# Kernel tuning notes

Hardware: AMD Instinct MI355X
Metric: run time of the kernel (lower is better)

The kernel has to match this reference:

```python
import jax, jax.numpy as jnp
import numpy as np

N, M = 8192, 1024  # n_frames, feature dim (input_size == output_size == 1024)
Q_SCALE = 0.06
DROP_P = 0.5


def setup_inputs() -> dict:
    key = jax.random.key(0)
    kx, kk, kq, kv, ko, ku = jax.random.split(key, 6)
    w_std = 0.02
    return {
        "x": jax.random.normal(kx, (N, M), dtype=jnp.float32),
        # nn.Linear stores weight as [out_features, in_features]
        "Wk": jax.random.normal(kk, (M, M), dtype=jnp.float32) * w_std,
        "Wq": jax.random.normal(kq, (M, M), dtype=jnp.float32) * w_std,
        "Wv": jax.random.normal(kv, (M, M), dtype=jnp.float32) * w_std,
        "Wo": jax.random.normal(ko, (M, M), dtype=jnp.float32) * w_std,
        # uniform noise for dropout mask on the [N, N] attention matrix
        "u": jax.random.uniform(ku, (N, N), dtype=jnp.float32),
    }


def reference(x, Wk, Wq, Wv, Wo, u):
    # projections (bias-free Linear: y = x @ W.T)
    K = x @ Wk.T                      # [N, M]
    Q = (x @ Wq.T) * Q_SCALE          # [N, M], Q *= 0.06
    V = x @ Wv.T                      # [N, M]
    logits = Q @ K.T                  # [N, N]
    attn = jax.nn.softmax(logits, axis=-1)
    # Dropout(p=0.5) in train mode: keep with prob 0.5, scale by 1/(1-p)=2
    keep = jnp.where(u >= DROP_P, jnp.float32(1.0 / (1.0 - DROP_P)), jnp.float32(0.0))
    w = attn * keep                   # [N, N]
    y = w @ V                         # [N, M]
    return y @ Wo.T                   # [N, M]
```

## Files before the change

### kernel.cpp

```cpp
#include <hip/hip_runtime.h>
#include <cstdint>
#include <cstddef>

#define NFRAMES 8192
#define MDIM    1024
#define Q_SCALE 0.06f

#define BK 64
#define BM2 256
#define BN2 256
#define BM 256
#define BN 128

typedef __bf16 bf16x8 __attribute__((ext_vector_type(8)));
typedef float  f32x4  __attribute__((ext_vector_type(4)));
typedef unsigned short us8 __attribute__((ext_vector_type(8)));

__device__ __forceinline__ unsigned short f2bf(float f) {
  union { float f; uint32_t u; } a; a.f = f;
  uint32_t u = a.u;
  u += 0x7FFFu + ((u >> 16) & 1u);
  return (unsigned short)(u >> 16);
}
__device__ __forceinline__ float bf2f(unsigned short h) {
  union { uint32_t u; float f; } a; a.u = ((uint32_t)h) << 16; return a.f;
}

__device__ __forceinline__ void async_ld16(const void* g, void* l) {
  __builtin_amdgcn_global_load_lds(
      (const __attribute__((address_space(1))) void*)(uintptr_t)g,
      (__attribute__((address_space(3))) void*)(uint32_t)(uintptr_t)l,
      16, 0, 0);
}

__device__ __forceinline__ void store_val(float* p, float v) { *p = v; }
__device__ __forceinline__ void store_val(unsigned short* p, float v) { *p = f2bf(v); }

template <typename OutT>
__global__ __launch_bounds__(512, 2) void gemm_big(
    const unsigned short* __restrict__ A, int lda,
    const unsigned short* __restrict__ B, int ldb,
    OutT* __restrict__ C, int ldc, long cz, int kChunk)
{
  __shared__ alignas(16) unsigned short As[2 * BM2 * BK];
  __shared__ alignas(16) unsigned short Bs[2 * BN2 * BK];

  const int tid  = threadIdx.x;
  const int wave = tid >> 6;
  const int lane = tid & 63;

  const int gX  = (int)gridDim.x;
  const int nwg = gX * (int)gridDim.y;
  int bx = (int)blockIdx.x, by = (int)blockIdx.y;
  if ((nwg & 7) == 0) {
    const int L  = by * gX + bx;
    const int qq = nwg >> 3;
    const int Ls = (L & 7) * qq + (L >> 3);
    bx = Ls % gX; by = Ls / gX;
  }

  const int m0 = by * BM2, n0 = bx * BN2;
  const int wm = (wave >> 2) * 128;
  const int wn = (wave & 3) * 64;
  const int fr = lane & 15, fq = lane >> 4;

  const int kOff = (int)blockIdx.z * kChunk;
  OutT* Cz = C + (size_t)blockIdx.z * cz;

  const int l8 = lane >> 3, l7 = lane & 7;
  const size_t ldaB = (size_t)lda * 2, ldbB = (size_t)ldb * 2;
  const char* aSrc = (const char*)A + (size_t)(m0 + wave * 8 + l8) * ldaB
                     + (size_t)kOff * 2 + ((l7 ^ l8) << 4);
  const char* bSrc = (const char*)B + (size_t)(n0 + wave * 8 + l8) * ldbB
                     + (size_t)kOff * 2 + ((l7 ^ l8) << 4);
  unsigned short* aDst = As + wave * 512;
  unsigned short* bDst = Bs + wave * 512;

  const int xorv = (fr & 7) << 4;
  const int c0 = (fq * 16) ^ xorv;
  const int c1 = (64 + fq * 16) ^ xorv;
  const char* aRd = (const char*)As + (wm + fr) * 128;
  const char* bRd = (const char*)Bs + (wn + fr) * 128;

  f32x4 acc[8][4] = {};
  const int NT = kChunk >> 6;

#define STA2(buf, s, t) async_ld16(aSrc + (size_t)((s) * 64) * ldaB + (size_t)(t) * 128, \
                                   aDst + (buf) * 16384 + (s) * 4096)
#define STB2(buf, s, t) async_ld16(bSrc + (size_t)((s) * 64) * ldbB + (size_t)(t) * 128, \
                                   bDst + (buf) * 16384 + (s) * 4096)

  STA2(0, 0, 0); STA2(0, 1, 0); STA2(0, 2, 0); STA2(0, 3, 0);
  STB2(0, 0, 0); STB2(0, 1, 0); STB2(0, 2, 0); STB2(0, 3, 0);
  asm volatile("s_waitcnt vmcnt(0)" ::: "memory");
  __builtin_amdgcn_s_barrier();

  for (int t = 0; t < NT; ++t) {
    const int cur = t & 1;
    const bool st = (t + 1 < NT);
    const char* aB = aRd + cur * 32768;
    const char* bB = bRd + cur * 32768;

    if (st) {
      const int u = t + 1, ub = cur ^ 1;
      STA2(ub, 0, u); STA2(ub, 1, u); STA2(ub, 2, u); STA2(ub, 3, u);
      STB2(ub, 0, u); STB2(ub, 1, u); STB2(ub, 2, u); STB2(ub, 3, u);
    }
    __builtin_amdgcn_sched_barrier(0);

    bf16x8 bh[4][2];
#pragma unroll
    for (int j = 0; j < 4; ++j) {
      bh[j][0] = *(const bf16x8*)(bB + j * 2048 + c0);
      bh[j][1] = *(const bf16x8*)(bB + j * 2048 + c1);
    }
    bf16x8 ar[2][2][2];
#pragma unroll
    for (int i = 0; i < 2; ++i) {
      ar[0][i][0] = *(const bf16x8*)(aB + i * 2048 + c0);
      ar[0][i][1] = *(const bf16x8*)(aB + i * 2048 + c1);
    }

#pragma unroll
    for (int ph = 0; ph < 4; ++ph) {
      const int pc = ph & 1, pn = pc ^ 1;
      if (ph < 3) {
#pragma unroll
        for (int i = 0; i < 2; ++i) {
          ar[pn][i][0] = *(const bf16x8*)(aB + (ph * 2 + 2 + i) * 2048 + c0);
          ar[pn][i][1] = *(const bf16x8*)(aB + (ph * 2 + 2 + i) * 2048 + c1);
        }
      }
      __builtin_amdgcn_s_setprio(1);
#pragma unroll
      for (int kk = 0; kk < 2; ++kk)
#pragma unroll
        for (int i = 0; i < 2; ++i)
#pragma unroll
          for (int j = 0; j < 4; ++j)
            acc[ph * 2 + i][j] = __builtin_amdgcn_mfma_f32_16x16x32_bf16(
                ar[pc][i][kk], bh[j][kk], acc[ph * 2 + i][j], 0, 0, 0);
      __builtin_amdgcn_s_setprio(0);
    }

    if (st) { asm volatile("s_waitcnt vmcnt(0)" ::: "memory"); }
    __builtin_amdgcn_s_barrier();
  }
#undef STA2
#undef STB2

#pragma unroll
  for (int mf = 0; mf < 8; ++mf)
#pragma unroll
    for (int nf = 0; nf < 4; ++nf)
#pragma unroll
      for (int r = 0; r < 4; ++r) {
        int row = m0 + wm + mf * 16 + fq * 4 + r;
        int col = n0 + wn + nf * 16 + fr;
        store_val(&Cz[(size_t)row * ldc + col], acc[mf][nf][r]);
      }
}

template <typename OutT>
__global__ __launch_bounds__(512, 2) void gemm_bt8(
    const unsigned short* __restrict__ A, int lda,
    const unsigned short* __restrict__ B, int ldb,
    OutT* __restrict__ C, int ldc, int K)
{
  __shared__ alignas(16) unsigned short As[3 * BM * BK];
  __shared__ alignas(16) unsigned short Bs[3 * BN * BK];

  const int tid  = threadIdx.x;
  const int wave = tid >> 6;
  const int lane = tid & 63;

  const int gX  = (int)gridDim.x;
  const int nwg = gX * (int)gridDim.y;
  const int L   = (int)blockIdx.y * gX + (int)blockIdx.x;
  const int qq  = nwg >> 3;
  const int Ls  = (L & 7) * qq + (L >> 3);
  const int bx  = Ls % gX, by = Ls / gX;

  const int m0 = by * BM, n0 = bx * BN;
  const int wm = (wave >> 1) * 64;
  const int wn = (wave & 1) * 64;
  const int fr = lane & 15, fq = lane >> 4;

  const int l8 = lane >> 3, l7 = lane & 7;
  const size_t ldaB = (size_t)lda * 2, ldbB = (size_t)ldb * 2;
  const char* aSrc = (const char*)A + (size_t)(m0 + wave * 8 + l8) * ldaB + ((l7 ^ l8) << 4);
  const char* bSrc = (const char*)B + (size_t)(n0 + wave * 8 + l8) * ldbB + ((l7 ^ l8) << 4);
  unsigned short* aDst = As + wave * 512;
  unsigned short* bDst = Bs + wave * 512;

  const int xorv = (fr & 7) << 4;
  const int cA0 = (fq * 16) ^ xorv;
  const int cA1 = (64 + fq * 16) ^ xorv;
  const char* aRd = (const char*)As + (wm + fr) * 128;
  const char* bRd = (const char*)Bs + (wn + fr) * 128;

  f32x4 acc[4][4] = {};
  const int NT = K >> 6;

#define STA(buf, s, t) async_ld16(aSrc + (size_t)((s) * 64) * ldaB + (size_t)(t) * 128, \
                                  aDst + (buf) * 16384 + (s) * 4096)
#define STB(buf, s, t) async_ld16(bSrc + (size_t)((s) * 64) * ldbB + (size_t)(t) * 128, \
                                  bDst + (buf) * 8192 + (s) * 4096)

  STA(0, 0, 0); STA(0, 1, 0); STA(0, 2, 0); STA(0, 3, 0); STB(0, 0, 0); STB(0, 1, 0);
  if (NT > 1) { STA(1, 0, 1); STA(1, 1, 1); STA(1, 2, 1); STA(1, 3, 1); STB(1, 0, 1); STB(1, 1, 1); }
  asm volatile("s_waitcnt vmcnt(6)" ::: "memory");
  __builtin_amdgcn_s_barrier();

  for (int t = 0; t < NT; ++t) {
    const int cur = t % 3;
    const int u   = t + 2;
    const int ub  = u % 3;
    const bool st = (u < NT);
    const char* aB = aRd + cur * 32768;
    const char* bB = bRd + cur * 16384;

    bf16x8 bh[4][2];
#pragma unroll
    for (int j = 0; j < 4; ++j) {
      bh[j][0] = *(const bf16x8*)(bB + j * 2048 + cA0);
      bh[j][1] = *(const bf16x8*)(bB + j * 2048 + cA1);
    }
    bf16x8 a0[2][2];
#pragma unroll
    for (int i = 0; i < 2; ++i) {
      a0[i][0] = *(const bf16x8*)(aB + i * 2048 + cA0);
      a0[i][1] = *(const bf16x8*)(aB + i * 2048 + cA1);
    }
    if (st) { STA(ub, 0, u); STA(ub, 1, u); STB(ub, 0, u); }
    __builtin_amdgcn_s_barrier();
    asm volatile("s_waitcnt lgkmcnt(0)" ::: "memory");
    __builtin_amdgcn_sched_barrier(0);
    __builtin_amdgcn_s_setprio(1);
#pragma unroll
    for (int kk = 0; kk < 2; ++kk)
#pragma unroll
      for (int i = 0; i < 2; ++i)
#pragma unroll
        for (int j = 0; j < 4; ++j)
          acc[i][j] = __builtin_amdgcn_mfma_f32_16x16x32_bf16(
              kk ? a0[i][1] : a0[i][0], kk ? bh[j][1] : bh[j][0], acc[i][j], 0, 0, 0);
    __builtin_amdgcn_s_setprio(0);
    __builtin_amdgcn_s_barrier();

    bf16x8 a1[2][2];
#pragma unroll
    for (int i = 0; i < 2; ++i) {
      a1[i][0] = *(const bf16x8*)(aB + (2 + i) * 2048 + cA0);
      a1[i][1] = *(const bf16x8*)(aB + (2 + i) * 2048 + cA1);
    }
    if (st) { STA(ub, 2, u); STA(ub, 3, u); STB(ub, 1, u); }
    if (st) { asm volatile("s_waitcnt vmcnt(6)" ::: "memory"); }
    else    { asm volatile("s_waitcnt vmcnt(0)" ::: "memory"); }
    __builtin_amdgcn_s_barrier();
    asm volatile("s_waitcnt lgkmcnt(0)" ::: "memory");
    __builtin_amdgcn_sched_barrier(0);
    __builtin_amdgcn_s_setprio(1);
#pragma unroll
    for (int kk = 0; kk < 2; ++kk)
#pragma unroll
      for (int i = 0; i < 2; ++i)
#pragma unroll
        for (int j = 0; j < 4; ++j)
          acc[2 + i][j] = __builtin_amdgcn_mfma_f32_16x16x32_bf16(
              kk ? a1[i][1] : a1[i][0], kk ? bh[j][1] : bh[j][0], acc[2 + i][j], 0, 0, 0);
    __builtin_amdgcn_s_setprio(0);
    __builtin_amdgcn_s_barrier();
  }
#undef STA
#undef STB

#pragma unroll
  for (int i = 0; i < 4; ++i)
#pragma unroll
    for (int j = 0; j < 4; ++j)
#pragma unroll
      for (int r = 0; r < 4; ++r) {
        int row = m0 + wm + i * 16 + fq * 4 + r;
        int col = n0 + wn + j * 16 + fr;
        store_val(&C[(size_t)row * ldc + col], acc[i][j][r]);
      }
}

__global__ __launch_bounds__(256) void softmax_dropout_kernel(
    const unsigned short* __restrict__ S, const float* __restrict__ U,
    unsigned short* __restrict__ P)
{
  const int row = blockIdx.x;
  const us8*   s8 = (const us8*)(S + (size_t)row * NFRAMES);
  const f32x4* u4 = (const f32x4*)(U + (size_t)row * NFRAMES);
  us8*         p8 = (us8*)(P + (size_t)row * NFRAMES);
  const int tid = threadIdx.x;
  const int lane = tid & 63, wave = tid >> 6;

  float v[32];
  float mx = -3.4e38f;
#pragma unroll
  for (int j = 0; j < 4; ++j) {
    us8 t = __builtin_nontemporal_load(s8 + j * 256 + tid);
#pragma unroll
    for (int e = 0; e < 8; ++e) {
      float f = bf2f(t[e]);
      v[j * 8 + e] = f;
      mx = fmaxf(mx, f);
    }
  }
#pragma unroll
  for (int o = 32; o > 0; o >>= 1) mx = fmaxf(mx, __shfl_xor(mx, o));
  __shared__ float redm[4];
  __shared__ float reds[4];
  if (lane == 0) redm[wave] = mx;
  __syncthreads();
  mx = fmaxf(fmaxf(redm[0], redm[1]), fmaxf(redm[2], redm[3]));

  float sum = 0.f;
#pragma unroll
  for (int i = 0; i < 32; ++i) { v[i] = __expf(v[i] - mx); sum += v[i]; }
#pragma unroll
  for (int o = 32; o > 0; o >>= 1) sum += __shfl_xor(sum, o);
  if (lane == 0) reds[wave] = sum;
  __syncthreads();
  sum = reds[0] + reds[1] + reds[2] + reds[3];
  float inv = 1.0f / sum;

#pragma unroll
  for (int j = 0; j < 4; ++j) {
    f32x4 ua = __builtin_nontemporal_load(u4 + (j * 256 + tid) * 2);
    f32x4 ub = __builtin_nontemporal_load(u4 + (j * 256 + tid) * 2 + 1);
    us8 o;
    o[0] = f2bf(v[j*8+0] * inv * (ua[0] >= 0.5f ? 2.0f : 0.0f));
    o[1] = f2bf(v[j*8+1] * inv * (ua[1] >= 0.5f ? 2.0f : 0.0f));
    o[2] = f2bf(v[j*8+2] * inv * (ua[2] >= 0.5f ? 2.0f : 0.0f));
    o[3] = f2bf(v[j*8+3] * inv * (ua[3] >= 0.5f ? 2.0f : 0.0f));
    o[4] = f2bf(v[j*8+4] * inv * (ub[0] >= 0.5f ? 2.0f : 0.0f));
    o[5] = f2bf(v[j*8+5] * inv * (ub[1] >= 0.5f ? 2.0f : 0.0f));
    o[6] = f2bf(v[j*8+6] * inv * (ub[2] >= 0.5f ? 2.0f : 0.0f));
    o[7] = f2bf(v[j*8+7] * inv * (ub[3] >= 0.5f ? 2.0f : 0.0f));
    p8[j * 256 + tid] = o;
  }
}

__device__ __forceinline__ void cvt4(const float* in, unsigned short* out, int i, float s) {
  float4 t = ((const float4*)in)[i];
  ushort4 o;
  o.x = f2bf(t.x * s); o.y = f2bf(t.y * s); o.z = f2bf(t.z * s); o.w = f2bf(t.w * s);
  ((ushort4*)out)[i] = o;
}

__global__ __launch_bounds__(256) void cvt_all(
    const float* __restrict__ x, const float* __restrict__ Wk,
    const float* __restrict__ Wq, const float* __restrict__ Wv,
    const float* __restrict__ Wo,
    unsigned short* __restrict__ xb, unsigned short* __restrict__ wkq,
    unsigned short* __restrict__ wvb, unsigned short* __restrict__ wob)
{
  int i = blockIdx.x * 256 + threadIdx.x;
  const int XSZ = (NFRAMES * MDIM) / 4;
  const int WSZ = (MDIM * MDIM) / 4;
  if (i < XSZ) { cvt4(x, xb, i, 1.0f); return; }
  i -= XSZ;
  if (i < WSZ) { cvt4(Wk, wkq, i, 1.0f); return; }
  i -= WSZ;
  if (i < WSZ) { cvt4(Wq, wkq + MDIM * MDIM, i, Q_SCALE); return; }
  i -= WSZ;
  if (i < WSZ) { cvt4(Wv, wvb, i, 1.0f); return; }
  i -= WSZ;
  if (i < WSZ) { cvt4(Wo, wob, i, 1.0f); return; }
}

__global__ __launch_bounds__(256) void reduce2_bf16(
    const float* __restrict__ Yp, long zs,
    unsigned short* __restrict__ out, int n4)
{
  int i = blockIdx.x * 256 + threadIdx.x;
  if (i < n4) {
    f32x4 a = __builtin_nontemporal_load((const f32x4*)Yp + i);
    f32x4 b = __builtin_nontemporal_load((const f32x4*)(Yp + zs) + i);
    ushort4 o;
    o.x = f2bf(a[0] + b[0]);
    o.y = f2bf(a[1] + b[1]);
    o.z = f2bf(a[2] + b[2]);
    o.w = f2bf(a[3] + b[3]);
    ((ushort4*)out)[i] = o;
  }
}

extern "C" void kernel_launch(void* const* d_in, const int* in_sizes, int n_in,
                              void* d_out, int out_size, void* d_ws, size_t ws_size,
                              hipStream_t stream) {
  const float* x  = (const float*)d_in[0];
  const float* Wk = (const float*)d_in[1];
  const float* Wq = (const float*)d_in[2];
  const float* Wv = (const float*)d_in[3];
  const float* Wo = (const float*)d_in[4];
  const float* u  = (const float*)d_in[5];
  float* out = (float*)d_out;

  const int N = NFRAMES, M = MDIM;
  char* base = (char*)d_ws;
  size_t off = 0;
  auto alloc = [&](size_t bytes) -> void* {
    void* p = base + off; off += (bytes + 255) & ~(size_t)255; return p;
  };
  unsigned short* xb  = (unsigned short*)alloc((size_t)N * M * 2);
  unsigned short* wkq = (unsigned short*)alloc((size_t)2 * M * M * 2);
  unsigned short* wvb = (unsigned short*)alloc((size_t)M * M * 2);
  unsigned short* wob = (unsigned short*)alloc((size_t)M * M * 2);
  unsigned short* KQb = (unsigned short*)alloc((size_t)N * 2 * M * 2);
  unsigned short* Vt  = (unsigned short*)alloc((size_t)M * N * 2);
  unsigned short* yb  = (unsigned short*)alloc((size_t)N * M * 2);

  size_t avail = ws_size > off ? ws_size - off : 0;
  int R = 256;
  const int cands[6] = {8192, 4096, 2048, 1024, 512, 256};
  for (int ci = 0; ci < 6; ++ci) {
    size_t need = (size_t)cands[ci] * N * 2 * 2 + 1024;
    if (need <= avail) { R = cands[ci]; break; }
  }
  unsigned short* Sb = (unsigned short*)alloc((size_t)R * N * 2);
  unsigned short* Pb = (unsigned short*)alloc((size_t)R * N * 2);
  float* Yp = (float*)Sb;

  {
    int total4 = (N * M + 4 * M * M) / 4;
    cvt_all<<<(total4 + 255) / 256, 256, 0, stream>>>(x, Wk, Wq, Wv, Wo, xb, wkq, wvb, wob);
  }

  gemm_big<unsigned short><<<dim3(2 * M / BN2, N / BM2), 512, 0, stream>>>(
      xb, M, wkq, M, KQb, 2 * M, 0, M);
  gemm_bt8<unsigned short><<<dim3(N / BN, M / BM), 512, 0, stream>>>(
      wvb, M, xb, M, Vt, N, M);

  for (int i0 = 0; i0 < N; i0 += R) {
    gemm_big<unsigned short><<<dim3(N / BN2, R / BM2), 512, 0, stream>>>(
        KQb + M + (size_t)i0 * 2 * M, 2 * M,
        KQb, 2 * M,
        Sb, N, 0, M);
    softmax_dropout_kernel<<<R, 256, 0, stream>>>(Sb, u + (size_t)i0 * N, Pb);
    gemm_big<float><<<dim3(M / BN2, R / BM2, 2), 512, 0, stream>>>(
        Pb, N, Vt, N, Yp, M, (long)R * M, N / 2);
    reduce2_bf16<<<(R * M / 4 + 255) / 256, 256, 0, stream>>>(
        Yp, (long)R * M, yb + (size_t)i0 * M, R * M / 4);
  }

  gemm_bt8<float><<<dim3(M / BN, N / BM), 512, 0, stream>>>(
      yb, M, wob, M, out, M, M);
}
```

Baseline: 716.8 us.

## Rewrite 256x256 GEMM main loop as 8-phase interleaved load/MFMA schedule

Replaces the double-buffered K loop of the big GEMM with an 8-phase schedule that unrolls two K tiles per iteration. Each phase issues part of the next tile's global-to-LDS loads, then runs a quarter of the MFMA block (4x2 fragments) between barriers. vmcnt(4) waits keep some prefetch in flight instead of draining it every tile. The goal is to overlap memory traffic with matrix math more finely, at the cost of many more barriers and an assumption that NT is even.

```diff
diff --git a/kernel.cpp b/kernel.cpp
--- a/kernel.cpp
+++ b/kernel.cpp
@@ -37,7 +37,7 @@
 __device__ __forceinline__ void store_val(unsigned short* p, float v) { *p = f2bf(v); }
 
 template <typename OutT>
-__global__ __launch_bounds__(512, 2) void gemm_big(
+__global__ __launch_bounds__(512, 2) void gemm_8ph(
     const unsigned short* __restrict__ A, int lda,
     const unsigned short* __restrict__ B, int ldb,
     OutT* __restrict__ C, int ldc, long cz, int kChunk)
@@ -73,81 +73,124 @@
                      + (size_t)kOff * 2 + ((l7 ^ l8) << 4);
   const char* bSrc = (const char*)B + (size_t)(n0 + wave * 8 + l8) * ldbB
                      + (size_t)kOff * 2 + ((l7 ^ l8) << 4);
-  unsigned short* aDst = As + wave * 512;
-  unsigned short* bDst = Bs + wave * 512;
 
   const int xorv = (fr & 7) << 4;
   const int c0 = (fq * 16) ^ xorv;
   const int c1 = (64 + fq * 16) ^ xorv;
   const char* aRd = (const char*)As + (wm + fr) * 128;
   const char* bRd = (const char*)Bs + (wn + fr) * 128;
+  const char* aB0 = aRd;
+  const char* aB1 = aRd + 32768;
+  const char* bB0 = bRd;
+  const char* bB1 = bRd + 32768;
 
   f32x4 acc[8][4] = {};
   const int NT = kChunk >> 6;
-
-#define STA2(buf, s, t) async_ld16(aSrc + (size_t)((s) * 64) * ldaB + (size_t)(t) * 128, \
-                                   aDst + (buf) * 16384 + (s) * 4096)
-#define STB2(buf, s, t) async_ld16(bSrc + (size_t)((s) * 64) * ldbB + (size_t)(t) * 128, \
-                                   bDst + (buf) * 16384 + (s) * 4096)
-
-  STA2(0, 0, 0); STA2(0, 1, 0); STA2(0, 2, 0); STA2(0, 3, 0);
-  STB2(0, 0, 0); STB2(0, 1, 0); STB2(0, 2, 0); STB2(0, 3, 0);
-  asm volatile("s_waitcnt vmcnt(0)" ::: "memory");
-  __builtin_amdgcn_s_barrier();
-
-  for (int t = 0; t < NT; ++t) {
-    const int cur = t & 1;
-    const bool st = (t + 1 < NT);
-    const char* aB = aRd + cur * 32768;
-    const char* bB = bRd + cur * 32768;
-
-    if (st) {
-      const int u = t + 1, ub = cur ^ 1;
-      STA2(ub, 0, u); STA2(ub, 1, u); STA2(ub, 2, u); STA2(ub, 3, u);
-      STB2(ub, 0, u); STB2(ub, 1, u); STB2(ub, 2, u); STB2(ub, 3, u);
-    }
-    __builtin_amdgcn_sched_barrier(0);
-
-    bf16x8 bh[4][2];
-#pragma unroll
-    for (int j = 0; j < 4; ++j) {
-      bh[j][0] = *(const bf16x8*)(bB + j * 2048 + c0);
-      bh[j][1] = *(const bf16x8*)(bB + j * 2048 + c1);
-    }
-    bf16x8 ar[2][2][2];
-#pragma unroll
-    for (int i = 0; i < 2; ++i) {
-      ar[0][i][0] = *(const bf16x8*)(aB + i * 2048 + c0);
-      ar[0][i][1] = *(const bf16x8*)(aB + i * 2048 + c1);
-    }
-
-#pragma unroll
-    for (int ph = 0; ph < 4; ++ph) {
-      const int pc = ph & 1, pn = pc ^ 1;
-      if (ph < 3) {
-#pragma unroll
-        for (int i = 0; i < 2; ++i) {
-          ar[pn][i][0] = *(const bf16x8*)(aB + (ph * 2 + 2 + i) * 2048 + c0);
-          ar[pn][i][1] = *(const bf16x8*)(aB + (ph * 2 + 2 + i) * 2048 + c1);
-        }
-      }
-      __builtin_amdgcn_s_setprio(1);
-#pragma unroll
-      for (int kk = 0; kk < 2; ++kk)
-#pragma unroll
-        for (int i = 0; i < 2; ++i)
-#pragma unroll
-          for (int j = 0; j < 4; ++j)
-            acc[ph * 2 + i][j] = __builtin_amdgcn_mfma_f32_16x16x32_bf16(
-                ar[pc][i][kk], bh[j][kk], acc[ph * 2 + i][j], 0, 0, 0);
-      __builtin_amdgcn_s_setprio(0);
-    }
-
-    if (st) { asm volatile("s_waitcnt vmcnt(0)" ::: "memory"); }
-    __builtin_amdgcn_s_barrier();
-  }
-#undef STA2
-#undef STB2
+  const int NI = NT >> 1;
+
+#define SA(b, h, t) do { \
+  async_ld16(aSrc + (size_t)((h) * 128)      * ldaB + (size_t)(t) * 128, \
+             As + (b) * 16384 + (h) * 8192 + wave * 512); \
+  async_ld16(aSrc + (size_t)((h) * 128 + 64) * ldaB + (size_t)(t) * 128, \
+             As + (b) * 16384 + (h) * 8192 + 4096 + wave * 512); \
+} while (0)
+#define SB(b, h, t) do { \
+  async_ld16(bSrc + (size_t)((h) * 128)      * ldbB + (size_t)(t) * 128, \
+             Bs + (b) * 16384 + (h) * 8192 + wave * 512); \
+  async_ld16(bSrc + (size_t)((h) * 128 + 64) * ldbB + (size_t)(t) * 128, \
+             Bs + (b) * 16384 + (h) * 8192 + 4096 + wave * 512); \
+} while (0)
+
+#define RD_A(dst, base, mh) do { \
+  _Pragma("unroll") \
+  for (int m_ = 0; m_ < 4; ++m_) { \
+    dst[m_][0] = *(const bf16x8*)((base) + ((mh) * 4 + m_) * 2048 + c0); \
+    dst[m_][1] = *(const bf16x8*)((base) + ((mh) * 4 + m_) * 2048 + c1); \
+  } \
+} while (0)
+#define RD_B(dst, base, nh) do { \
+  _Pragma("unroll") \
+  for (int n_ = 0; n_ < 2; ++n_) { \
+    dst[n_][0] = *(const bf16x8*)((base) + ((nh) * 2 + n_) * 2048 + c0); \
+    dst[n_][1] = *(const bf16x8*)((base) + ((nh) * 2 + n_) * 2048 + c1); \
+  } \
+} while (0)
+
+#define BARR() __builtin_amdgcn_s_barrier()
+#define LGKM0() do { asm volatile("s_waitcnt lgkmcnt(0)" ::: "memory"); \
+                     __builtin_amdgcn_sched_barrier(0); } while (0)
+#define MM(mh, nh, af, bf) do { \
+  __builtin_amdgcn_s_setprio(1); \
+  _Pragma("unroll") \
+  for (int kk_ = 0; kk_ < 2; ++kk_) \
+  _Pragma("unroll") \
+  for (int m_ = 0; m_ < 4; ++m_) \
+  _Pragma("unroll") \
+  for (int n_ = 0; n_ < 2; ++n_) \
+    acc[(mh) * 4 + m_][(nh) * 2 + n_] = __builtin_amdgcn_mfma_f32_16x16x32_bf16( \
+        af[m_][kk_], bf[n_][kk_], acc[(mh) * 4 + m_][(nh) * 2 + n_], 0, 0, 0); \
+  __builtin_amdgcn_s_setprio(0); \
+} while (0)
+
+#define BODY(G, T1) do { \
+  bf16x8 aF[4][2], bF0[2][2], bF1[2][2]; \
+   \
+  RD_A(aF, aB0, 0); RD_B(bF0, bB0, 0); \
+  SA(1, 0, (T1)); \
+  BARR(); LGKM0(); MM(0, 0, aF, bF0); BARR(); \
+   \
+  RD_B(bF1, bB0, 1); \
+  SA(1, 1, (T1)); \
+  BARR(); LGKM0(); MM(0, 1, aF, bF1); BARR(); \
+   \
+  RD_A(aF, aB0, 1); \
+  if (G) SB(0, 0, (T1) + 1); \
+  BARR(); LGKM0(); MM(1, 0, aF, bF0); BARR(); \
+   \
+  if (G) SB(0, 1, (T1) + 1); \
+  BARR(); MM(1, 1, aF, bF1); \
+  if (G) { asm volatile("s_waitcnt vmcnt(4)" ::: "memory"); } \
+  else   { asm volatile("s_waitcnt vmcnt(0)" ::: "memory"); } \
+  BARR(); __builtin_amdgcn_sched_barrier(0); \
+   \
+  RD_A(aF, aB1, 0); RD_B(bF0, bB1, 0); \
+  if (G) SA(0, 0, (T1) + 1); \
+  BARR(); LGKM0(); MM(0, 0, aF, bF0); BARR(); \
+   \
+  RD_B(bF1, bB1, 1); \
+  if (G) SA(0, 1, (T1) + 1); \
+  BARR(); LGKM0(); MM(0, 1, aF, bF1); BARR(); \
+   \
+  RD_A(aF, aB1, 1); \
+  if (G) SB(1, 0, (T1) + 2); \
+  BARR(); LGKM0(); MM(1, 0, aF, bF0); BARR(); \
+   \
+  if (G) SB(1, 1, (T1) + 2); \
+  BARR(); MM(1, 1, aF, bF1); \
+  if (G) { asm volatile("s_waitcnt vmcnt(4)" ::: "memory"); } \
+  BARR(); __builtin_amdgcn_sched_barrier(0); \
+} while (0)
+
+  SA(0, 0, 0); SA(0, 1, 0);
+  SB(0, 0, 0); SB(0, 1, 0);
+  SB(1, 0, 1); SB(1, 1, 1);
+  asm volatile("s_waitcnt vmcnt(4)" ::: "memory");
+  BARR();
+  __builtin_amdgcn_sched_barrier(0);
+
+  for (int i = 0; i + 1 < NI; ++i) {
+    BODY(true, 2 * i + 1);
+  }
+  BODY(false, NT - 1);
+
+#undef SA
+#undef SB
+#undef RD_A
+#undef RD_B
+#undef BARR
+#undef LGKM0
+#undef MM
+#undef BODY
 
 #pragma unroll
   for (int mf = 0; mf < 8; ++mf)
@@ -431,18 +474,18 @@
     cvt_all<<<(total4 + 255) / 256, 256, 0, stream>>>(x, Wk, Wq, Wv, Wo, xb, wkq, wvb, wob);
   }
 
-  gemm_big<unsigned short><<<dim3(2 * M / BN2, N / BM2), 512, 0, stream>>>(
+  gemm_8ph<unsigned short><<<dim3(2 * M / BN2, N / BM2), 512, 0, stream>>>(
       xb, M, wkq, M, KQb, 2 * M, 0, M);
   gemm_bt8<unsigned short><<<dim3(N / BN, M / BM), 512, 0, stream>>>(
       wvb, M, xb, M, Vt, N, M);
 
   for (int i0 = 0; i0 < N; i0 += R) {
-    gemm_big<unsigned short><<<dim3(N / BN2, R / BM2), 512, 0, stream>>>(
+    gemm_8ph<unsigned short><<<dim3(N / BN2, R / BM2), 512, 0, stream>>>(
         KQb + M + (size_t)i0 * 2 * M, 2 * M,
         KQb, 2 * M,
         Sb, N, 0, M);
     softmax_dropout_kernel<<<R, 256, 0, stream>>>(Sb, u + (size_t)i0 * N, Pb);
-    gemm_big<float><<<dim3(M / BN2, R / BM2, 2), 512, 0, stream>>>(
+    gemm_8ph<float><<<dim3(M / BN2, R / BM2, 2), 512, 0, stream>>>(
         Pb, N, Vt, N, Yp, M, (long)R * M, N / 2);
     reduce2_bf16<<<(R * M / 4 + 255) / 256, 256, 0, stream>>>(
         Yp, (long)R * M, yb + (size_t)i0 * M, R * M / 4);
```

New measurement: 722.4 us. About the same (+0.8%).
